# Kernel optimization log

Measured on AMD Instinct MI355X. Metric: run time of the kernel, lower is better.

The kernel has to match this reference:

```python
import math
import jax, jax.numpy as jnp
import numpy as np

N, C_S, C_Z, C, H, PQK, PV = 768, 384, 128, 16, 12, 4, 8
INF, EPS = 100000.0, 1e-8


def _quat_to_rot(q):
    # q: [N,4] normalized quaternions -> [N,3,3] rotation matrices
    w, x, y, z = q[:, 0], q[:, 1], q[:, 2], q[:, 3]
    return jnp.stack([
        jnp.stack([1 - 2 * (y * y + z * z), 2 * (x * y - w * z), 2 * (x * z + w * y)], -1),
        jnp.stack([2 * (x * y + w * z), 1 - 2 * (x * x + z * z), 2 * (y * z - w * x)], -1),
        jnp.stack([2 * (x * z - w * y), 2 * (y * z + w * x), 1 - 2 * (x * x + y * y)], -1),
    ], -2)


def setup_inputs() -> dict:
    key = jax.random.key(0)
    ks = jax.random.split(key, 16)
    quat = jax.random.normal(ks[2], (N, 4))
    quat = quat / jnp.linalg.norm(quat, axis=-1, keepdims=True)
    sc = 0.02
    return {
        "s": jax.random.normal(ks[0], (N, C_S), jnp.float32),
        "z": jax.random.normal(ks[1], (N, N, C_Z), jnp.float32),
        "rot": _quat_to_rot(quat).astype(jnp.float32),
        "trans": jax.random.normal(ks[3], (N, 3), jnp.float32),
        "mask": jnp.ones((N,), jnp.float32),
        "Wq": sc * jax.random.normal(ks[4], (C_S, H * C), jnp.float32),
        "bq": jnp.zeros((H * C,), jnp.float32),
        "Wqp": sc * jax.random.normal(ks[5], (C_S, H * 3 * PQK), jnp.float32),
        "bqp": jnp.zeros((H * 3 * PQK,), jnp.float32),
        "Wkv": sc * jax.random.normal(ks[6], (C_S, 2 * H * C), jnp.float32),
        "bkv": jnp.zeros((2 * H * C,), jnp.float32),
        "Wkvp": sc * jax.random.normal(ks[7], (C_S, H * 3 * (PQK + PV)), jnp.float32),
        "bkvp": jnp.zeros((H * 3 * (PQK + PV),), jnp.float32),
        "Wb": sc * jax.random.normal(ks[8], (C_Z, H), jnp.float32),
        "bb": jnp.zeros((H,), jnp.float32),
        "head_weights": 0.5413 * jnp.ones((H,), jnp.float32),  # softplus^{-1}(1)
        "Wout": sc * jax.random.normal(ks[9], (H * (C_Z + C + PV * 4), C_S), jnp.float32),
        "bout": jnp.zeros((C_S,), jnp.float32),
    }


def _proj_points(x, W, b, rot, trans, P):
    # PointProjection: split last dim into 3 coord chunks, stack as last axis
    pl = x @ W + b                                   # [N, H*3*P]
    pl = pl.reshape(-1, 3, H * P).transpose(0, 2, 1).reshape(-1, H, P, 3)
    return jnp.einsum('nij,nhpj->nhpi', rot, pl) + trans[:, None, None, :]


def reference(s, z, rot, trans, mask, Wq, bq, Wqp, bqp, Wkv, bkv, Wkvp, bkvp,
              Wb, bb, head_weights, Wout, bout):
    q = (s @ Wq + bq).reshape(N, H, C)
    kv = (s @ Wkv + bkv).reshape(N, H, 2 * C)
    k, v = kv[..., :C], kv[..., C:]
    q_pts = _proj_points(s, Wqp, bqp, rot, trans, PQK)          # [N,H,PQK,3]
    kv_pts = _proj_points(s, Wkvp, bkvp, rot, trans, PQK + PV)  # [N,H,PQK+PV,3]
    k_pts, v_pts = kv_pts[..., :PQK, :], kv_pts[..., PQK:, :]

    b_bias = z @ Wb + bb                                        # [N,N,H]
    a = jnp.einsum('qhc,khc->hqk', q, k) * math.sqrt(1.0 / (3 * C))
    a = a + math.sqrt(1.0 / 3) * jnp.transpose(b_bias, (2, 0, 1))

    # point-distance attention: [q,k,H,PQK]
    d2 = jnp.sum((q_pts[:, None] - k_pts[None]) ** 2, axis=-1)
    hw = jax.nn.softplus(head_weights) * math.sqrt(1.0 / (3 * (PQK * 9.0 / 2)))
    pt_att = -0.5 * jnp.sum(d2 * hw[:, None], axis=-1)          # [q,k,H]
    a = a + jnp.transpose(pt_att, (2, 0, 1))

    sq_mask = INF * (mask[:, None] * mask[None, :] - 1.0)       # [q,k]
    a = jax.nn.softmax(a + sq_mask[None], axis=-1)              # [H,q,k]

    o = jnp.einsum('hqk,khc->qhc', a, v).reshape(N, H * C)
    o_pt = jnp.einsum('hqk,khpd->qhpd', a, v_pts)               # [q,H,PV,3]
    o_pt = jnp.einsum('nji,nhpj->nhpi', rot, o_pt - trans[:, None, None, :])  # invert_apply
    o_pt_norm = jnp.sqrt(jnp.sum(o_pt ** 2, -1) + EPS).reshape(N, H * PV)
    o_pt_flat = o_pt.reshape(N, H * PV, 3)
    o_pair = jnp.einsum('hqk,qkc->qhc', a, z).reshape(N, H * C_Z)

    cat = jnp.concatenate(
        [o, o_pt_flat[..., 0], o_pt_flat[..., 1], o_pt_flat[..., 2], o_pt_norm, o_pair], -1)
    return cat @ Wout + bout
```

## Files before the change

kernel.cpp:

```cpp
#include <hip/hip_runtime.h>
#include <math.h>

#define NN    768
#define CS    384
#define INF_  100000.0f

typedef __attribute__((ext_vector_type(8))) short s16x8;
typedef __attribute__((ext_vector_type(4))) float f32x4;

#define OFF_Q       0
#define OFF_K       147456
#define OFF_V       294912
#define OFF_QPRAW   442368
#define OFF_KVPRAW  552960
#define OFF_QPTS    884736
#define OFF_KPTS    995328
#define OFF_VPTS    1105920
#define OFF_KT      1327104
#define OFF_KPT     1474560
#define OFF_CAT     8414208

__device__ __forceinline__ unsigned short f2bf(float x) {
  unsigned u = __float_as_uint(x) + 0x8000u;
  return (unsigned short)(u >> 16);
}
__device__ __forceinline__ unsigned pk2(float a, float b) {
  return (unsigned)f2bf(a) | ((unsigned)f2bf(b) << 16);
}

__global__ void __launch_bounds__(256)
k1_proj(const float* __restrict__ s,
        const float* __restrict__ Wq,  const float* __restrict__ bq,
        const float* __restrict__ Wqp, const float* __restrict__ bqp,
        const float* __restrict__ Wkv, const float* __restrict__ bkv,
        const float* __restrict__ Wkvp,const float* __restrict__ bkvp,
        float* __restrict__ ws) {
  __shared__ float s_lds[8][CS];
  const int n0 = blockIdx.y * 8;
  const int j0 = blockIdx.x * 32;
  const int t  = threadIdx.x;

  const float4* s4  = (const float4*)(s + (size_t)n0 * CS);
  float4*       sl4 = (float4*)(&s_lds[0][0]);
  for (int i = t; i < 768; i += 256) sl4[i] = s4[i];
  __syncthreads();

  const int m = t >> 5;
  const int j = j0 + (t & 31);

  const float* W; const float* bv; int jj, ncols;
  if (j < 192)      { W = Wq;   bv = bq;   jj = j;       ncols = 192; }
  else if (j < 576) { W = Wkv;  bv = bkv;  jj = j - 192; ncols = 384; }
  else if (j < 720) { W = Wqp;  bv = bqp;  jj = j - 576; ncols = 144; }
  else              { W = Wkvp; bv = bkvp; jj = j - 720; ncols = 432; }

  float acc = bv[jj];
  const float* Wp = W + jj;
  for (int c = 0; c < CS; ++c) acc += s_lds[m][c] * Wp[(size_t)c * ncols];

  const int n = n0 + m;
  if (j < 192) {
    (ws + OFF_Q)[n * 192 + jj] = acc;
  } else if (j < 576) {
    int h = jj >> 5, c = jj & 31;
    if (c < 16) (ws + OFF_K)[n * 192 + h * 16 + c] = acc;
    else        (ws + OFF_V)[n * 192 + h * 16 + (c - 16)] = acc;
  } else if (j < 720) {
    (ws + OFF_QPRAW)[n * 144 + jj] = acc;
  } else {
    (ws + OFF_KVPRAW)[n * 432 + jj] = acc;
  }
}

__global__ void __launch_bounds__(256)
k2_rot(const float* __restrict__ rot, const float* __restrict__ trans,
       float* __restrict__ ws) {
  const int idx = blockIdx.x * 256 + threadIdx.x;
  const int n = idx / 192;
  const int r = idx % 192;
  const float* R = rot + n * 9;
  const float* T = trans + n * 3;
  if (r < 48) {
    const float* raw = ws + OFF_QPRAW + n * 144;
    float p0 = raw[r], p1 = raw[48 + r], p2 = raw[96 + r];
    float g0 = R[0]*p0 + R[1]*p1 + R[2]*p2 + T[0];
    float g1 = R[3]*p0 + R[4]*p1 + R[5]*p2 + T[1];
    float g2 = R[6]*p0 + R[7]*p1 + R[8]*p2 + T[2];
    float* qp = ws + OFF_QPTS + n * 144 + r * 3;
    qp[0] = g0; qp[1] = g1; qp[2] = g2;
  } else {
    const int r2 = r - 48;
    const float* raw = ws + OFF_KVPRAW + n * 432;
    float p0 = raw[r2], p1 = raw[144 + r2], p2 = raw[288 + r2];
    float g0 = R[0]*p0 + R[1]*p1 + R[2]*p2 + T[0];
    float g1 = R[3]*p0 + R[4]*p1 + R[5]*p2 + T[1];
    float g2 = R[6]*p0 + R[7]*p1 + R[8]*p2 + T[2];
    const int h = r2 / 12, p = r2 % 12;
    if (p < 4) {
      float* kp = ws + OFF_KPTS + n * 144 + (h * 4 + p) * 3;
      kp[0] = g0; kp[1] = g1; kp[2] = g2;
    } else {
      float* vp = ws + OFF_VPTS + n * 288 + (h * 8 + (p - 4)) * 3;
      vp[0] = g0; vp[1] = g1; vp[2] = g2;
    }
  }
}

__global__ void __launch_bounds__(256)
k2b_tr(float* __restrict__ ws) {
  const int i = blockIdx.x * 256 + threadIdx.x;
  if (i < 147456) {
    const int n = i / 192, cc = i % 192;
    (ws + OFF_KT)[cc * 768 + n] = (ws + OFF_K)[i];
  } else {
    const int i2 = i - 147456;
    const int n = i2 / 144, r = i2 % 144;
    (ws + OFF_KPT)[r * 768 + n] = (ws + OFF_KPTS)[i2];
  }
}

#define ZT_S 72
#define ZR_S 136
#define WT_S 72
#define WH_S 68
__global__ void __launch_bounds__(256, 3)
k3_fused(const float* __restrict__ z, const float* __restrict__ rot,
         const float* __restrict__ trans, const float* __restrict__ mask,
         const float* __restrict__ Wb, const float* __restrict__ bb,
         const float* __restrict__ hwin, float* __restrict__ ws) {
  const int q = blockIdx.x, t = threadIdx.x;
  const int g   = t >> 6;
  const int kl  = t & 63;
  const int l15 = kl & 15, lq = kl >> 4;

  __shared__ unsigned short zT[128 * ZT_S];
  __shared__ unsigned short zR[64 * ZR_S];
  __shared__ unsigned short wT[16 * WT_S];
  __shared__ float wH[12 * WH_S];
  __shared__ float bias_s[64 * 13];
  __shared__ float hw_l[12], bb_l[12], lsum[12], linv[12];
  __shared__ float opt_raw[288];

  if (t < 12) {
    hw_l[t] = logf(1.0f + expf(hwin[t])) * 0.13608276348795434f;
    bb_l[t] = bb[t];
  }

  s16x8 wbA[4];
  #pragma unroll
  for (int kk = 0; kk < 4; ++kk) {
    #pragma unroll
    for (int j = 0; j < 8; ++j) {
      float v = (l15 < 12) ? Wb[(kk * 32 + lq * 8 + j) * 12 + l15] : 0.0f;
      wbA[kk][j] = (short)f2bf(v);
    }
  }

  const float maskq  = mask[q];
  const float* qrow  = ws + OFF_Q    + q * 192;
  const float* qprow = ws + OFF_QPTS + q * 144;
  const float* ktr   = ws + OFF_KT;
  const float* kptr  = ws + OFF_KPT;
  const float* vbase = ws + OFF_V;
  const float* vpbase= ws + OFF_VPTS;
  const float4* zg4  = (const float4*)z + (size_t)q * 24576;

  float l3[3] = {0.f, 0.f, 0.f};
  f32x4 opA = {0.f,0.f,0.f,0.f}, opB = {0.f,0.f,0.f,0.f};
  float o_acc = 0.f;
  float pt0 = 0.f, pt1 = 0.f;
  const int oh  = t >> 4;
  const int ph  = t / 24,        prr = t % 24;
  const int p2s = 256 + t, p2h = p2s / 24;

  for (int k0 = 0; k0 < NN; k0 += 64) {
    __syncthreads();

    float4 zv[8];
    #pragma unroll
    for (int j = 0; j < 8; ++j) zv[j] = zg4[k0 * 32 + t + 256 * j];
    const int kb = t >> 5, c4 = t & 31;
    #pragma unroll
    for (int j = 0; j < 8; ++j) {
      uint2 d;
      d.x = pk2(zv[j].x, zv[j].y);
      d.y = pk2(zv[j].z, zv[j].w);
      *(uint2*)&zR[(kb + 8 * j) * ZR_S + c4 * 4] = d;
    }
    #pragma unroll
    for (int e = 0; e < 4; ++e) {
      uint4 d;
      d.x = pk2(((const float*)&zv[0])[e], ((const float*)&zv[1])[e]);
      d.y = pk2(((const float*)&zv[2])[e], ((const float*)&zv[3])[e]);
      d.z = pk2(((const float*)&zv[4])[e], ((const float*)&zv[5])[e]);
      d.w = pk2(((const float*)&zv[6])[e], ((const float*)&zv[7])[e]);
      *(uint4*)&zT[(c4 * 4 + e) * ZT_S + kb * 8] = d;
    }
    __syncthreads();

    {
      f32x4 bd = {0.f,0.f,0.f,0.f};
      #pragma unroll
      for (int kk = 0; kk < 4; ++kk) {
        s16x8 bf = *(const s16x8*)&zR[(g * 16 + l15) * ZR_S + kk * 32 + lq * 8];
        bd = __builtin_amdgcn_mfma_f32_16x16x32_bf16(wbA[kk], bf, bd, 0, 0, 0);
      }
      #pragma unroll
      for (int r = 0; r < 4; ++r) {
        const int h = lq * 4 + r;
        if (h < 12) bias_s[(g * 16 + l15) * 13 + h] = bd[r];
      }
    }
    float lg[3];
    {
      const int kg = k0 + kl;
      const float mterm = INF_ * (maskq * mask[kg] - 1.0f);
      #pragma unroll
      for (int j = 0; j < 3; ++j) {
        const int h = g + 4 * j;
        float qk = 0.f;
        #pragma unroll
        for (int c = 0; c < 16; ++c)
          qk += qrow[h * 16 + c] * ktr[(h * 16 + c) * 768 + kg];
        float pt = 0.f;
        #pragma unroll
        for (int r = 0; r < 12; ++r) {
          const float d = qprow[h * 12 + r] - kptr[(h * 12 + r) * 768 + kg];
          pt += d * d;
        }
        lg[j] = 0.14433756729740643f * qk
              + 0.57735026918962576f * bb_l[h]
              - 0.5f * hw_l[h] * pt + mterm;
      }
    }
    __syncthreads();

    #pragma unroll
    for (int j = 0; j < 3; ++j) {
      const int h = g + 4 * j;
      const float wv = __expf(lg[j] + 0.57735026918962576f * bias_s[kl * 13 + h]);
      l3[j] += wv;
      wH[h * WH_S + kl] = wv;
      wT[h * WT_S + (((kl & 7) << 3) | (kl >> 3))] = f2bf(wv);
    }
    __syncthreads();

    #pragma unroll
    for (int kk = 0; kk < 2; ++kk) {
      s16x8 af = *(const s16x8*)&wT[l15 * WT_S + kk * 32 + lq * 8];
      s16x8 b0 = *(const s16x8*)&zT[((2 * g)     * 16 + l15) * ZT_S + kk * 32 + lq * 8];
      opA = __builtin_amdgcn_mfma_f32_16x16x32_bf16(af, b0, opA, 0, 0, 0);
      s16x8 b1 = *(const s16x8*)&zT[((2 * g + 1) * 16 + l15) * ZT_S + kk * 32 + lq * 8];
      opB = __builtin_amdgcn_mfma_f32_16x16x32_bf16(af, b1, opB, 0, 0, 0);
    }
    {
      const float* vpr = vpbase + (size_t)k0 * 288;
      const float* vr  = vbase  + (size_t)k0 * 192;
      #pragma unroll 4
      for (int k4 = 0; k4 < 16; ++k4) {
        const int k = k4 * 4;
        {
          const float4 w4 = *(const float4*)&wH[ph * WH_S + k];
          pt0 += w4.x * vpr[(k    ) * 288 + t] + w4.y * vpr[(k + 1) * 288 + t]
               + w4.z * vpr[(k + 2) * 288 + t] + w4.w * vpr[(k + 3) * 288 + t];
        }
        if (t < 32) {
          const float4 w4 = *(const float4*)&wH[p2h * WH_S + k];
          pt1 += w4.x * vpr[(k    ) * 288 + p2s] + w4.y * vpr[(k + 1) * 288 + p2s]
               + w4.z * vpr[(k + 2) * 288 + p2s] + w4.w * vpr[(k + 3) * 288 + p2s];
        }
        if (t < 192) {
          const float4 w4 = *(const float4*)&wH[oh * WH_S + k];
          o_acc += w4.x * vr[(k    ) * 192 + t] + w4.y * vr[(k + 1) * 192 + t]
                 + w4.z * vr[(k + 2) * 192 + t] + w4.w * vr[(k + 3) * 192 + t];
        }
      }
    }
  }

  #pragma unroll
  for (int j = 0; j < 3; ++j) {
    float v = l3[j];
    for (int off = 1; off < 64; off <<= 1) v += __shfl_xor(v, off, 64);
    l3[j] = v;
  }
  if (kl == 0) { lsum[g] = l3[0]; lsum[g + 4] = l3[1]; lsum[g + 8] = l3[2]; }
  __syncthreads();
  if (t < 12) linv[t] = 1.0f / lsum[t];
  __syncthreads();

  float* cat = ws + OFF_CAT + (size_t)q * 2112;
  #pragma unroll
  for (int r = 0; r < 4; ++r) {
    const int h = lq * 4 + r;
    if (h < 12) {
      cat[576 + h * 128 + (2 * g)     * 16 + l15] = opA[r] * linv[h];
      cat[576 + h * 128 + (2 * g + 1) * 16 + l15] = opB[r] * linv[h];
    }
  }
  if (t < 192) cat[t] = o_acc * linv[oh];
  opt_raw[t] = pt0 * linv[ph];
  if (t < 32) opt_raw[p2s] = pt1 * linv[p2h];
  __syncthreads();

  if (t < 96) {
    const int h = t >> 3, p = t & 7;
    const float* R = rot + q * 9;
    const float* T = trans + q * 3;
    const float g0 = opt_raw[h * 24 + p * 3 + 0] - T[0];
    const float g1 = opt_raw[h * 24 + p * 3 + 1] - T[1];
    const float g2 = opt_raw[h * 24 + p * 3 + 2] - T[2];
    const float x  = R[0]*g0 + R[3]*g1 + R[6]*g2;
    const float y  = R[1]*g0 + R[4]*g1 + R[7]*g2;
    const float zc = R[2]*g0 + R[5]*g1 + R[8]*g2;
    const int hp = h * 8 + p;
    cat[192 + hp] = x;
    cat[288 + hp] = y;
    cat[384 + hp] = zc;
    cat[480 + hp] = sqrtf(x*x + y*y + zc*zc + 1e-8f);
  }
}

__global__ void __launch_bounds__(256)
k5_init(const float* __restrict__ bout, float* __restrict__ out) {
  const int i = blockIdx.x * 256 + threadIdx.x;
  out[i] = bout[i % 384];
}

#define K5_CH 48
__global__ void __launch_bounds__(256)
k5_out(const float* __restrict__ Wout, const float* __restrict__ ws,
       float* __restrict__ out) {
  __shared__ float At[K5_CH * 68];
  __shared__ float Bn[K5_CH * 68];
  const int n0  = blockIdx.x * 64;
  const int m0  = blockIdx.y * 64;
  const int ks0 = blockIdx.z * 528;
  const int t = threadIdx.x;
  const int tx = t & 15, ty = t >> 4;
  float acc[4][4] = {{0.f}};

  const float* catg = ws + OFF_CAT;
  for (int kc = 0; kc < 528; kc += K5_CH) {
    __syncthreads();
    #pragma unroll
    for (int ii = 0; ii < 12; ++ii) {
      const int i = t + 256 * ii;
      const int m = i / 48, k = i % 48;
      At[k * 68 + m] = catg[(size_t)(m0 + m) * 2112 + ks0 + kc + k];
    }
    #pragma unroll
    for (int ii = 0; ii < 12; ++ii) {
      const int i = t + 256 * ii;
      const int k = i >> 6, n = i & 63;
      Bn[k * 68 + n] = Wout[(size_t)(ks0 + kc + k) * 384 + n0 + n];
    }
    __syncthreads();
    #pragma unroll 4
    for (int k = 0; k < K5_CH; ++k) {
      const float4 a4 = *(const float4*)&At[k * 68 + ty * 4];
      const float4 b4 = *(const float4*)&Bn[k * 68 + tx * 4];
      acc[0][0] += a4.x * b4.x; acc[0][1] += a4.x * b4.y; acc[0][2] += a4.x * b4.z; acc[0][3] += a4.x * b4.w;
      acc[1][0] += a4.y * b4.x; acc[1][1] += a4.y * b4.y; acc[1][2] += a4.y * b4.z; acc[1][3] += a4.y * b4.w;
      acc[2][0] += a4.z * b4.x; acc[2][1] += a4.z * b4.y; acc[2][2] += a4.z * b4.z; acc[2][3] += a4.z * b4.w;
      acc[3][0] += a4.w * b4.x; acc[3][1] += a4.w * b4.y; acc[3][2] += a4.w * b4.z; acc[3][3] += a4.w * b4.w;
    }
  }
  #pragma unroll
  for (int r = 0; r < 4; ++r)
    #pragma unroll
    for (int c = 0; c < 4; ++c)
      atomicAdd(&out[(size_t)(m0 + ty * 4 + r) * 384 + n0 + tx * 4 + c], acc[r][c]);
}

extern "C" void kernel_launch(void* const* d_in, const int* in_sizes, int n_in,
                              void* d_out, int out_size, void* d_ws, size_t ws_size,
                              hipStream_t stream) {
  const float* s     = (const float*)d_in[0];
  const float* z     = (const float*)d_in[1];
  const float* rot   = (const float*)d_in[2];
  const float* trans = (const float*)d_in[3];
  const float* mask  = (const float*)d_in[4];
  const float* Wq    = (const float*)d_in[5];
  const float* bq    = (const float*)d_in[6];
  const float* Wqp   = (const float*)d_in[7];
  const float* bqp   = (const float*)d_in[8];
  const float* Wkv   = (const float*)d_in[9];
  const float* bkv   = (const float*)d_in[10];
  const float* bkvp_w= (const float*)d_in[11];
  const float* bkvp  = (const float*)d_in[12];
  const float* Wb    = (const float*)d_in[13];
  const float* bb    = (const float*)d_in[14];
  const float* hw    = (const float*)d_in[15];
  const float* Wout  = (const float*)d_in[16];
  const float* bout  = (const float*)d_in[17];
  float* out = (float*)d_out;
  float* ws  = (float*)d_ws;

  k1_proj<<<dim3(36, 96), 256, 0, stream>>>(s, Wq, bq, Wqp, bqp, Wkv, bkv, bkvp_w, bkvp, ws);
  k2_rot <<<576, 256, 0, stream>>>(rot, trans, ws);
  k2b_tr <<<1008, 256, 0, stream>>>(ws);
  k3_fused<<<NN, 256, 0, stream>>>(z, rot, trans, mask, Wb, bb, hw, ws);
  k5_init<<<1152, 256, 0, stream>>>(bout, out);
  k5_out<<<dim3(6, 12, 4), 256, 0, stream>>>(Wout, ws, out);
}
```

Before: 837.8 us.

## Precompute pair bias in separate pass, retile projection and output GEMMs

Adds a kb_bias kernel that computes the z·Wb pair bias for every (q,k) pair in FP32 and stores it as bf16 in the workspace. k3_fused then reads this bias instead of running MFMA on a row-major bf16 copy of z, which removes the zR LDS buffer and one barrier per tile and raises the occupancy hint from 3 to 6. The z tile load into zT is split into halves with a rotated write order to reduce LDS conflicts. k1_proj becomes a tiled LDS GEMM and k5_out is retiled with a different split-K, at the cost of reading z an extra time and writing an extra bias buffer to global memory.

```diff
diff --git a/kernel.cpp b/kernel.cpp
--- a/kernel.cpp
+++ b/kernel.cpp
@@ -18,6 +18,7 @@
 #define OFF_VPTS    1105920
 #define OFF_KT      1327104
 #define OFF_KPT     1474560
+#define OFF_BIAS    1585152
 #define OFF_CAT     8414208
 
 __device__ __forceinline__ unsigned short f2bf(float x) {
@@ -26,6 +27,9 @@
 }
 __device__ __forceinline__ unsigned pk2(float a, float b) {
   return (unsigned)f2bf(a) | ((unsigned)f2bf(b) << 16);
+}
+__device__ __forceinline__ float bf2f(unsigned short u) {
+  return __uint_as_float(((unsigned)u) << 16);
 }
 
 __global__ void __launch_bounds__(256)
@@ -35,40 +39,70 @@
         const float* __restrict__ Wkv, const float* __restrict__ bkv,
         const float* __restrict__ Wkvp,const float* __restrict__ bkvp,
         float* __restrict__ ws) {
-  __shared__ float s_lds[8][CS];
-  const int n0 = blockIdx.y * 8;
-  const int j0 = blockIdx.x * 32;
+  const int n0 = blockIdx.x * 16;
+  const int m0 = blockIdx.y * 128;
   const int t  = threadIdx.x;
 
-  const float4* s4  = (const float4*)(s + (size_t)n0 * CS);
-  float4*       sl4 = (float4*)(&s_lds[0][0]);
-  for (int i = t; i < 768; i += 256) sl4[i] = s4[i];
-  __syncthreads();
-
-  const int m = t >> 5;
-  const int j = j0 + (t & 31);
-
-  const float* W; const float* bv; int jj, ncols;
-  if (j < 192)      { W = Wq;   bv = bq;   jj = j;       ncols = 192; }
-  else if (j < 576) { W = Wkv;  bv = bkv;  jj = j - 192; ncols = 384; }
-  else if (j < 720) { W = Wqp;  bv = bqp;  jj = j - 576; ncols = 144; }
-  else              { W = Wkvp; bv = bkvp; jj = j - 720; ncols = 432; }
-
-  float acc = bv[jj];
-  const float* Wp = W + jj;
-  for (int c = 0; c < CS; ++c) acc += s_lds[m][c] * Wp[(size_t)c * ncols];
-
-  const int n = n0 + m;
-  if (j < 192) {
-    (ws + OFF_Q)[n * 192 + jj] = acc;
-  } else if (j < 576) {
-    int h = jj >> 5, c = jj & 31;
-    if (c < 16) (ws + OFF_K)[n * 192 + h * 16 + c] = acc;
-    else        (ws + OFF_V)[n * 192 + h * 16 + (c - 16)] = acc;
-  } else if (j < 720) {
-    (ws + OFF_QPRAW)[n * 144 + jj] = acc;
-  } else {
-    (ws + OFF_KVPRAW)[n * 432 + jj] = acc;
+  const float* W; const float* bv; int base, ncols;
+  if (n0 < 192)      { W = Wq;   bv = bq;   base = 0;   ncols = 192; }
+  else if (n0 < 576) { W = Wkv;  bv = bkv;  base = 192; ncols = 384; }
+  else if (n0 < 720) { W = Wqp;  bv = bqp;  base = 576; ncols = 144; }
+  else               { W = Wkvp; bv = bkvp; base = 720; ncols = 432; }
+  const int jj0 = n0 - base;
+
+  __shared__ float As[32 * 130];
+  __shared__ float Bs[32 * 20];
+  const int tx = t & 3, ty = t >> 2;
+  float acc[2][4] = {{0.f}};
+
+  for (int kc = 0; kc < CS; kc += 32) {
+    __syncthreads();
+    #pragma unroll
+    for (int jj = 0; jj < 4; ++jj) {
+      const int idx = t + 256 * jj;
+      const int row = idx >> 3, c4 = idx & 7;
+      const float4 v = *(const float4*)&s[(size_t)(m0 + row) * CS + kc + c4 * 4];
+      As[(c4 * 4 + 0) * 130 + row] = v.x;
+      As[(c4 * 4 + 1) * 130 + row] = v.y;
+      As[(c4 * 4 + 2) * 130 + row] = v.z;
+      As[(c4 * 4 + 3) * 130 + row] = v.w;
+    }
+    if (t < 128) {
+      const int row = t >> 2, c4 = t & 3;
+      const float4 v = *(const float4*)&W[(size_t)(kc + row) * ncols + jj0 + c4 * 4];
+      *(float4*)&Bs[row * 20 + c4 * 4] = v;
+    }
+    __syncthreads();
+    #pragma unroll 8
+    for (int k = 0; k < 32; ++k) {
+      const float2 a2 = *(const float2*)&As[k * 130 + ty * 2];
+      const float4 b4 = *(const float4*)&Bs[k * 20 + tx * 4];
+      acc[0][0] += a2.x * b4.x; acc[0][1] += a2.x * b4.y;
+      acc[0][2] += a2.x * b4.z; acc[0][3] += a2.x * b4.w;
+      acc[1][0] += a2.y * b4.x; acc[1][1] += a2.y * b4.y;
+      acc[1][2] += a2.y * b4.z; acc[1][3] += a2.y * b4.w;
+    }
+  }
+
+  #pragma unroll
+  for (int r = 0; r < 2; ++r) {
+    const int n = m0 + ty * 2 + r;
+    #pragma unroll
+    for (int e = 0; e < 4; ++e) {
+      const int j = n0 + tx * 4 + e;
+      const float val = acc[r][e] + bv[j - base];
+      if (j < 192) {
+        (ws + OFF_Q)[n * 192 + j] = val;
+      } else if (j < 576) {
+        const int jj = j - 192, h = jj >> 5, c = jj & 31;
+        if (c < 16) (ws + OFF_K)[n * 192 + h * 16 + c] = val;
+        else        (ws + OFF_V)[n * 192 + h * 16 + (c - 16)] = val;
+      } else if (j < 720) {
+        (ws + OFF_QPRAW)[n * 144 + (j - 576)] = val;
+      } else {
+        (ws + OFF_KVPRAW)[n * 432 + (j - 720)] = val;
+      }
+    }
   }
 }
 
@@ -119,25 +153,70 @@
   }
 }
 
+__global__ void __launch_bounds__(256)
+kb_bias(const float* __restrict__ z, const float* __restrict__ Wb,
+        float* __restrict__ ws) {
+  const int row0 = blockIdx.x * 64;
+  const int t = threadIdx.x;
+  __shared__ float4 z4[64 * 32];
+  __shared__ float part[4 * 64 * 13];
+
+  const float4* zg = (const float4*)z + (size_t)row0 * 32;
+  {
+    const int kb = t >> 5, c4 = t & 31;
+    #pragma unroll
+    for (int j = 0; j < 8; ++j) {
+      const int row = kb + 8 * j;
+      z4[row * 32 + (c4 ^ (row & 31))] = zg[(size_t)row * 32 + c4];
+    }
+  }
+  __syncthreads();
+  {
+    const int r = t & 63, cq = t >> 6;
+    float acc[12];
+    #pragma unroll
+    for (int h = 0; h < 12; ++h) acc[h] = 0.f;
+    #pragma unroll
+    for (int i = 0; i < 8; ++i) {
+      const int c4l = cq * 8 + i;
+      const float4 v = z4[r * 32 + (c4l ^ (r & 31))];
+      const float* wb = Wb + c4l * 48;
+      #pragma unroll
+      for (int h = 0; h < 12; ++h)
+        acc[h] += v.x * wb[h] + v.y * wb[12 + h] + v.z * wb[24 + h] + v.w * wb[36 + h];
+    }
+    #pragma unroll
+    for (int h = 0; h < 12; ++h) part[(cq * 64 + r) * 13 + h] = acc[h];
+  }
+  __syncthreads();
+  {
+    const int r2 = t & 63, hg = t >> 6;
+    unsigned short* bg = (unsigned short*)(ws + OFF_BIAS);
+    #pragma unroll
+    for (int e = 0; e < 3; ++e) {
+      const int h = hg * 3 + e;
+      const float v = part[(0 * 64 + r2) * 13 + h] + part[(1 * 64 + r2) * 13 + h]
+                    + part[(2 * 64 + r2) * 13 + h] + part[(3 * 64 + r2) * 13 + h];
+      bg[(size_t)h * 589824 + row0 + r2] = f2bf(v);
+    }
+  }
+}
+
 #define ZT_S 72
-#define ZR_S 136
 #define WT_S 72
 #define WH_S 68
-__global__ void __launch_bounds__(256, 3)
+__global__ void __launch_bounds__(256, 6)
 k3_fused(const float* __restrict__ z, const float* __restrict__ rot,
          const float* __restrict__ trans, const float* __restrict__ mask,
-         const float* __restrict__ Wb, const float* __restrict__ bb,
-         const float* __restrict__ hwin, float* __restrict__ ws) {
+         const float* __restrict__ bb, const float* __restrict__ hwin,
+         float* __restrict__ ws) {
   const int q = blockIdx.x, t = threadIdx.x;
-  const int g   = t >> 6;
-  const int kl  = t & 63;
+  const int g = t >> 6, kl = t & 63;
   const int l15 = kl & 15, lq = kl >> 4;
 
   __shared__ unsigned short zT[128 * ZT_S];
-  __shared__ unsigned short zR[64 * ZR_S];
   __shared__ unsigned short wT[16 * WT_S];
   __shared__ float wH[12 * WH_S];
-  __shared__ float bias_s[64 * 13];
   __shared__ float hw_l[12], bb_l[12], lsum[12], linv[12];
   __shared__ float opt_raw[288];
 
@@ -146,72 +225,44 @@
     bb_l[t] = bb[t];
   }
 
-  s16x8 wbA[4];
-  #pragma unroll
-  for (int kk = 0; kk < 4; ++kk) {
-    #pragma unroll
-    for (int j = 0; j < 8; ++j) {
-      float v = (l15 < 12) ? Wb[(kk * 32 + lq * 8 + j) * 12 + l15] : 0.0f;
-      wbA[kk][j] = (short)f2bf(v);
-    }
-  }
-
-  const float maskq  = mask[q];
+  const float maskq = mask[q];
   const float* qrow  = ws + OFF_Q    + q * 192;
   const float* qprow = ws + OFF_QPTS + q * 144;
   const float* ktr   = ws + OFF_KT;
   const float* kptr  = ws + OFF_KPT;
   const float* vbase = ws + OFF_V;
   const float* vpbase= ws + OFF_VPTS;
+  const unsigned short* bgr = (const unsigned short*)(ws + OFF_BIAS);
   const float4* zg4  = (const float4*)z + (size_t)q * 24576;
 
   float l3[3] = {0.f, 0.f, 0.f};
   f32x4 opA = {0.f,0.f,0.f,0.f}, opB = {0.f,0.f,0.f,0.f};
-  float o_acc = 0.f;
-  float pt0 = 0.f, pt1 = 0.f;
-  const int oh  = t >> 4;
-  const int ph  = t / 24,        prr = t % 24;
+  float o_acc = 0.f, pt0 = 0.f, pt1 = 0.f;
+  const int oh = t >> 4;
+  const int ph = t / 24;
   const int p2s = 256 + t, p2h = p2s / 24;
 
   for (int k0 = 0; k0 < NN; k0 += 64) {
     __syncthreads();
 
-    float4 zv[8];
-    #pragma unroll
-    for (int j = 0; j < 8; ++j) zv[j] = zg4[k0 * 32 + t + 256 * j];
     const int kb = t >> 5, c4 = t & 31;
     #pragma unroll
-    for (int j = 0; j < 8; ++j) {
-      uint2 d;
-      d.x = pk2(zv[j].x, zv[j].y);
-      d.y = pk2(zv[j].z, zv[j].w);
-      *(uint2*)&zR[(kb + 8 * j) * ZR_S + c4 * 4] = d;
-    }
-    #pragma unroll
-    for (int e = 0; e < 4; ++e) {
-      uint4 d;
-      d.x = pk2(((const float*)&zv[0])[e], ((const float*)&zv[1])[e]);
-      d.y = pk2(((const float*)&zv[2])[e], ((const float*)&zv[3])[e]);
-      d.z = pk2(((const float*)&zv[4])[e], ((const float*)&zv[5])[e]);
-      d.w = pk2(((const float*)&zv[6])[e], ((const float*)&zv[7])[e]);
-      *(uint4*)&zT[(c4 * 4 + e) * ZT_S + kb * 8] = d;
-    }
-    __syncthreads();
-
-    {
-      f32x4 bd = {0.f,0.f,0.f,0.f};
+    for (int half = 0; half < 2; ++half) {
+      float4 zv[4];
       #pragma unroll
-      for (int kk = 0; kk < 4; ++kk) {
-        s16x8 bf = *(const s16x8*)&zR[(g * 16 + l15) * ZR_S + kk * 32 + lq * 8];
-        bd = __builtin_amdgcn_mfma_f32_16x16x32_bf16(wbA[kk], bf, bd, 0, 0, 0);
+      for (int j = 0; j < 4; ++j)
+        zv[j] = zg4[(size_t)(k0 + kb + 8 * (half * 4 + j)) * 32 + c4];
+      #pragma unroll
+      for (int w = 0; w < 4; ++w) {
+        const int e = ((c4 >> 1) + w) & 3;
+        uint2 d;
+        d.x = pk2(((const float*)&zv[0])[e], ((const float*)&zv[1])[e]);
+        d.y = pk2(((const float*)&zv[2])[e], ((const float*)&zv[3])[e]);
+        *(uint2*)&zT[(c4 * 4 + e) * ZT_S + kb * 8 + half * 4] = d;
       }
-      #pragma unroll
-      for (int r = 0; r < 4; ++r) {
-        const int h = lq * 4 + r;
-        if (h < 12) bias_s[(g * 16 + l15) * 13 + h] = bd[r];
-      }
-    }
-    float lg[3];
+    }
+    __syncthreads();
+
     {
       const int kg = k0 + kl;
       const float mterm = INF_ * (maskq * mask[kg] - 1.0f);
@@ -228,20 +279,15 @@
           const float d = qprow[h * 12 + r] - kptr[(h * 12 + r) * 768 + kg];
           pt += d * d;
         }
-        lg[j] = 0.14433756729740643f * qk
-              + 0.57735026918962576f * bb_l[h]
-              - 0.5f * hw_l[h] * pt + mterm;
+        const float bias = bf2f(bgr[(size_t)h * 589824 + (size_t)q * 768 + kg]);
+        const float logit = 0.14433756729740643f * qk
+                          + 0.57735026918962576f * (bias + bb_l[h])
+                          - 0.5f * hw_l[h] * pt + mterm;
+        const float wv = __expf(logit);
+        l3[j] += wv;
+        wH[h * WH_S + kl] = wv;
+        wT[h * WT_S + ((kl & 7) * 8 + (kl >> 3))] = f2bf(wv);
       }
-    }
-    __syncthreads();
-
-    #pragma unroll
-    for (int j = 0; j < 3; ++j) {
-      const int h = g + 4 * j;
-      const float wv = __expf(lg[j] + 0.57735026918962576f * bias_s[kl * 13 + h]);
-      l3[j] += wv;
-      wH[h * WH_S + kl] = wv;
-      wT[h * WT_S + (((kl & 7) << 3) | (kl >> 3))] = f2bf(wv);
     }
     __syncthreads();
 
@@ -327,50 +373,53 @@
   out[i] = bout[i % 384];
 }
 
-#define K5_CH 48
 __global__ void __launch_bounds__(256)
 k5_out(const float* __restrict__ Wout, const float* __restrict__ ws,
        float* __restrict__ out) {
-  __shared__ float At[K5_CH * 68];
-  __shared__ float Bn[K5_CH * 68];
-  const int n0  = blockIdx.x * 64;
-  const int m0  = blockIdx.y * 64;
-  const int ks0 = blockIdx.z * 528;
+  const int n0  = blockIdx.x * 16;
+  const int m0  = blockIdx.y * 128;
+  const int ks0 = blockIdx.z * 352;
   const int t = threadIdx.x;
-  const int tx = t & 15, ty = t >> 4;
-  float acc[4][4] = {{0.f}};
+
+  __shared__ float As[32 * 130];
+  __shared__ float Bs[32 * 20];
+  const int tx = t & 3, ty = t >> 2;
+  float acc[2][4] = {{0.f}};
 
   const float* catg = ws + OFF_CAT;
-  for (int kc = 0; kc < 528; kc += K5_CH) {
-    __syncthreads();
-    #pragma unroll
-    for (int ii = 0; ii < 12; ++ii) {
-      const int i = t + 256 * ii;
-      const int m = i / 48, k = i % 48;
-      At[k * 68 + m] = catg[(size_t)(m0 + m) * 2112 + ks0 + kc + k];
-    }
-    #pragma unroll
-    for (int ii = 0; ii < 12; ++ii) {
-      const int i = t + 256 * ii;
-      const int k = i >> 6, n = i & 63;
-      Bn[k * 68 + n] = Wout[(size_t)(ks0 + kc + k) * 384 + n0 + n];
-    }
-    __syncthreads();
-    #pragma unroll 4
-    for (int k = 0; k < K5_CH; ++k) {
-      const float4 a4 = *(const float4*)&At[k * 68 + ty * 4];
-      const float4 b4 = *(const float4*)&Bn[k * 68 + tx * 4];
-      acc[0][0] += a4.x * b4.x; acc[0][1] += a4.x * b4.y; acc[0][2] += a4.x * b4.z; acc[0][3] += a4.x * b4.w;
-      acc[1][0] += a4.y * b4.x; acc[1][1] += a4.y * b4.y; acc[1][2] += a4.y * b4.z; acc[1][3] += a4.y * b4.w;
-      acc[2][0] += a4.z * b4.x; acc[2][1] += a4.z * b4.y; acc[2][2] += a4.z * b4.z; acc[2][3] += a4.z * b4.w;
-      acc[3][0] += a4.w * b4.x; acc[3][1] += a4.w * b4.y; acc[3][2] += a4.w * b4.z; acc[3][3] += a4.w * b4.w;
+  for (int kc = 0; kc < 352; kc += 32) {
+    __syncthreads();
+    #pragma unroll
+    for (int jj = 0; jj < 4; ++jj) {
+      const int idx = t + 256 * jj;
+      const int row = idx >> 3, c4 = idx & 7;
+      const float4 v = *(const float4*)&catg[(size_t)(m0 + row) * 2112 + ks0 + kc + c4 * 4];
+      As[(c4 * 4 + 0) * 130 + row] = v.x;
+      As[(c4 * 4 + 1) * 130 + row] = v.y;
+      As[(c4 * 4 + 2) * 130 + row] = v.z;
+      As[(c4 * 4 + 3) * 130 + row] = v.w;
+    }
+    if (t < 128) {
+      const int row = t >> 2, c4 = t & 3;
+      const float4 v = *(const float4*)&Wout[(size_t)(ks0 + kc + row) * 384 + n0 + c4 * 4];
+      *(float4*)&Bs[row * 20 + c4 * 4] = v;
+    }
+    __syncthreads();
+    #pragma unroll 8
+    for (int k = 0; k < 32; ++k) {
+      const float2 a2 = *(const float2*)&As[k * 130 + ty * 2];
+      const float4 b4 = *(const float4*)&Bs[k * 20 + tx * 4];
+      acc[0][0] += a2.x * b4.x; acc[0][1] += a2.x * b4.y;
+      acc[0][2] += a2.x * b4.z; acc[0][3] += a2.x * b4.w;
+      acc[1][0] += a2.y * b4.x; acc[1][1] += a2.y * b4.y;
+      acc[1][2] += a2.y * b4.z; acc[1][3] += a2.y * b4.w;
     }
   }
   #pragma unroll
-  for (int r = 0; r < 4; ++r)
-    #pragma unroll
-    for (int c = 0; c < 4; ++c)
-      atomicAdd(&out[(size_t)(m0 + ty * 4 + r) * 384 + n0 + tx * 4 + c], acc[r][c]);
+  for (int r = 0; r < 2; ++r)
+    #pragma unroll
+    for (int e = 0; e < 4; ++e)
+      atomicAdd(&out[(size_t)(m0 + ty * 2 + r) * 384 + n0 + tx * 4 + e], acc[r][e]);
 }
 
 extern "C" void kernel_launch(void* const* d_in, const int* in_sizes, int n_in,
@@ -387,7 +436,7 @@
   const float* bqp   = (const float*)d_in[8];
   const float* Wkv   = (const float*)d_in[9];
   const float* bkv   = (const float*)d_in[10];
-  const float* bkvp_w= (const float*)d_in[11];
+  const float* Wkvp  = (const float*)d_in[11];
   const float* bkvp  = (const float*)d_in[12];
   const float* Wb    = (const float*)d_in[13];
   const float* bb    = (const float*)d_in[14];
@@ -397,10 +446,11 @@
   float* out = (float*)d_out;
   float* ws  = (float*)d_ws;
 
-  k1_proj<<<dim3(36, 96), 256, 0, stream>>>(s, Wq, bq, Wqp, bqp, Wkv, bkv, bkvp_w, bkvp, ws);
+  kb_bias<<<9216, 256, 0, stream>>>(z, Wb, ws);
+  k1_proj<<<dim3(72, 6), 256, 0, stream>>>(s, Wq, bq, Wqp, bqp, Wkv, bkv, Wkvp, bkvp, ws);
   k2_rot <<<576, 256, 0, stream>>>(rot, trans, ws);
   k2b_tr <<<1008, 256, 0, stream>>>(ws);
-  k3_fused<<<NN, 256, 0, stream>>>(z, rot, trans, mask, Wb, bb, hw, ws);
+  k3_fused<<<NN, 256, 0, stream>>>(z, rot, trans, mask, bb, hw, ws);
   k5_init<<<1152, 256, 0, stream>>>(bout, out);
-  k5_out<<<dim3(6, 12, 4), 256, 0, stream>>>(Wout, ws, out);
-}
+  k5_out<<<dim3(24, 6, 6), 256, 0, stream>>>(Wout, ws, out);
+}
```

Result: slower. 1.086 ms (+29.6%).
